# Kernel tuning notes

Measured on AMD Instinct MI355X. Metric: run time of the kernel, lower is better.

## Reference

```python
import jax, jax.numpy as jnp
import numpy as np

N_NODES = 50000


def graph_conv(src, dst, x, W, b, n_nodes):
    """DGL GraphConv, norm='both': D_out^{-1/2} A D_in^{-1/2} x W + b.
    src/dst: [E] edge endpoints (message flows src -> dst).
    """
    ones = jnp.ones(src.shape[0], dtype=x.dtype)
    deg_out = jnp.clip(jax.ops.segment_sum(ones, src, num_segments=n_nodes), 1.0)
    deg_in = jnp.clip(jax.ops.segment_sum(ones, dst, num_segments=n_nodes), 1.0)
    h = x * jax.lax.rsqrt(deg_out)[:, None]          # src-side normalization
    msgs = h[src]                                     # [E, F] gather (irregular)
    agg = jax.ops.segment_sum(msgs, dst, num_segments=n_nodes)  # SpMM scatter-add
    agg = agg * jax.lax.rsqrt(deg_in)[:, None]        # dst-side normalization
    return agg @ W + b


def setup_inputs() -> dict:
    key = jax.random.key(0)
    ks = jax.random.split(key, 9)
    E = 600000
    in_f, hid, emb = 128, 64, 32
    features = jax.random.normal(ks[0], (N_NODES, in_f), dtype=jnp.float32)
    src = jax.random.randint(ks[1], (E,), 0, N_NODES)
    dst = jax.random.randint(ks[2], (E,), 0, N_NODES)

    def glorot(k, fan_in, fan_out):
        lim = np.sqrt(6.0 / (fan_in + fan_out)).astype(np.float32)
        return jax.random.uniform(k, (fan_in, fan_out), jnp.float32, -lim, lim)

    return {
        "features": features, "src": src, "dst": dst,
        "W1": glorot(ks[3], in_f, hid), "b1": jnp.zeros((hid,), jnp.float32),
        "W2": glorot(ks[4], hid, emb), "b2": jnp.zeros((emb,), jnp.float32),
        "W3": glorot(ks[5], emb, in_f), "b3": jnp.zeros((in_f,), jnp.float32),
    }


def reference(features, src, dst, W1, b1, W2, b2, W3, b3):
    h = jax.nn.relu(graph_conv(src, dst, features, W1, b1, N_NODES))
    z = graph_conv(src, dst, h, W2, b2, N_NODES)
    recon = graph_conv(src, dst, z, W3, b3, N_NODES)
    return (z, recon)
```

## Files before the change

### kernel.cpp

```cpp
#include <hip/hip_runtime.h>
#include <hip/hip_bf16.h>


#define NN   50000
#define HPB  128
#define FNB  4
#define FBIN 12500
typedef unsigned short u16;

__device__ __forceinline__ float bfhi(unsigned u) {
    unsigned v = u & 0xFFFF0000u;
    return __builtin_bit_cast(float, v);
}
__device__ __forceinline__ float bflo(unsigned u) {
    unsigned v = u << 16;
    return __builtin_bit_cast(float, v);
}
__device__ __forceinline__ unsigned f2bf(float f) {
    unsigned u = __builtin_bit_cast(unsigned, f);
    return (u + 0x7FFFu + ((u >> 16) & 1u)) >> 16;
}

__global__ __launch_bounds__(256) void k_hist1(
    const int* __restrict__ src, const int* __restrict__ dst,
    u16* __restrict__ slab, int E, int slice)
{
    __shared__ unsigned h[NN / 2];
    const int which = blockIdx.x / HPB;
    const int p     = blockIdx.x % HPB;
    const int* __restrict__ idx = which ? dst : src;

    for (int i = threadIdx.x; i < NN / 2; i += 256) h[i] = 0;
    __syncthreads();

    const int beg = p * slice;
    const int fin = min(beg + slice, E);
    for (int i = beg + threadIdx.x * 4; i + 3 < fin; i += 1024) {
        const int4 v = *(const int4*)(idx + i);
        atomicAdd(&h[v.x >> 1], 1u << ((v.x & 1) << 4));
        atomicAdd(&h[v.y >> 1], 1u << ((v.y & 1) << 4));
        atomicAdd(&h[v.z >> 1], 1u << ((v.z & 1) << 4));
        atomicAdd(&h[v.w >> 1], 1u << ((v.w & 1) << 4));
    }
    for (int i = beg + ((fin - beg) & ~3) + threadIdx.x; i < fin; i += 256) {
        const int u = idx[i];
        atomicAdd(&h[u >> 1], 1u << ((u & 1) << 4));
    }
    __syncthreads();

    unsigned* out = (unsigned*)(slab + (size_t)blockIdx.x * NN);
    for (int i = threadIdx.x; i < NN / 2; i += 256) out[i] = h[i];
}

__global__ __launch_bounds__(256) void k_reduce_scan(
    u16* __restrict__ slab, float* __restrict__ rs_out, float* __restrict__ rs_in,
    int* __restrict__ partial, int* __restrict__ blocksum, int N)
{
    __shared__ int tmp[256];
    const int tid = threadIdx.x;
    const int i = blockIdx.x * 256 + tid;

    int run = 0;
    if (i < N) {
        const u16* s_src = slab + i;
        u16*       s_dst = slab + (size_t)HPB * NN + i;
        int so = 0;
#pragma unroll 8
        for (int p = 0; p < HPB; ++p) so += s_src[(size_t)p * NN];
#pragma unroll 8
        for (int p = 0; p < HPB; ++p) {
            const int c = s_dst[(size_t)p * NN];
            s_dst[(size_t)p * NN] = (u16)run;
            run += c;
        }
        rs_out[i] = rsqrtf(fmaxf((float)so, 1.0f));
        rs_in[i]  = rsqrtf(fmaxf((float)run, 1.0f));
    }
    tmp[tid] = run; __syncthreads();
    for (int off = 1; off < 256; off <<= 1) {
        int t = (tid >= off) ? tmp[tid - off] : 0;
        __syncthreads(); tmp[tid] += t; __syncthreads();
    }
    if (i < N) partial[i] = tmp[tid];
    if (tid == 255) blocksum[blockIdx.x] = tmp[255];
}

__global__ __launch_bounds__(256) void k_scan23(
    const int* __restrict__ partial, const int* __restrict__ blocksum,
    int* __restrict__ row_ptr, int n, int nb)
{
    __shared__ int tmp[256];
    const int tid = threadIdx.x;
    int v = (tid < nb) ? blocksum[tid] : 0;
    tmp[tid] = v; __syncthreads();
    for (int off = 1; off < 256; off <<= 1) {
        int t = (tid >= off) ? tmp[tid - off] : 0;
        __syncthreads(); tmp[tid] += t; __syncthreads();
    }
    __syncthreads();
    const int i = blockIdx.x * 256 + tid;
    if (i < n) {
        const int base = (blockIdx.x > 0) ? tmp[blockIdx.x - 1] : 0;
        row_ptr[i + 1] = partial[i] + base;
        if (i == 0) row_ptr[0] = 0;
    }
}

__global__ __launch_bounds__(256) void k_fill2(
    const int* __restrict__ src, const int* __restrict__ dst,
    const int* __restrict__ row_ptr, const u16* __restrict__ slab,
    int* __restrict__ csr_src, int E, int slice, int N)
{
    __shared__ int cur[FBIN];
    const int bin = blockIdx.x / HPB;
    const int p   = blockIdx.x % HPB;
    const int lo  = bin * FBIN;

    const u16* part_off = slab + (size_t)(HPB + p) * NN;
    for (int j = threadIdx.x; j < FBIN; j += 256) {
        const int node = lo + j;
        cur[j] = (node < N) ? (row_ptr[node] + (int)part_off[node]) : 0;
    }
    __syncthreads();

    const int beg = p * slice;
    const int fin = min(beg + slice, E);
    for (int i = beg + threadIdx.x * 4; i + 3 < fin; i += 1024) {
        const int4 d = *(const int4*)(dst + i);
        const int4 s = *(const int4*)(src + i);
        int u;
        u = d.x - lo; if ((unsigned)u < (unsigned)FBIN) csr_src[atomicAdd(&cur[u], 1)] = s.x;
        u = d.y - lo; if ((unsigned)u < (unsigned)FBIN) csr_src[atomicAdd(&cur[u], 1)] = s.y;
        u = d.z - lo; if ((unsigned)u < (unsigned)FBIN) csr_src[atomicAdd(&cur[u], 1)] = s.z;
        u = d.w - lo; if ((unsigned)u < (unsigned)FBIN) csr_src[atomicAdd(&cur[u], 1)] = s.w;
    }
    for (int i = beg + ((fin - beg) & ~3) + threadIdx.x; i < fin; i += 256) {
        int u = dst[i] - lo;
        if ((unsigned)u < (unsigned)FBIN) csr_src[atomicAdd(&cur[u], 1)] = src[i];
    }
}

template <int IN_F, int OUT_F, int TM>
__global__ __launch_bounds__(256) void k_gemm_bf16out(
    const float* __restrict__ X, const float* __restrict__ W,
    const float* __restrict__ rowscale, u16* __restrict__ Y, int n)
{
    constexpr int CT  = OUT_F / 4;
    constexpr int RT  = 256 / CT;
    constexpr int RPT = TM / RT;
    constexpr int XS  = IN_F + 4;
    __shared__ float sW[IN_F * OUT_F];
    __shared__ float sX[TM * XS];
    const int tid = threadIdx.x;
    const int row0 = blockIdx.x * TM;

    for (int i = tid; i < IN_F * OUT_F / 4; i += 256)
        ((float4*)sW)[i] = ((const float4*)W)[i];
    for (int i = tid; i < TM * IN_F / 4; i += 256) {
        const int r  = i / (IN_F / 4);
        const int c4 = (i % (IN_F / 4)) * 4;
        const int gr = row0 + r;
        float4 v = make_float4(0.f, 0.f, 0.f, 0.f);
        if (gr < n) v = *(const float4*)(X + (long)gr * IN_F + c4);
        *(float4*)(sX + r * XS + c4) = v;
    }
    __syncthreads();

    const int tc = tid % CT;
    const int tr = tid / CT;
    float4 acc[RPT];
#pragma unroll
    for (int i = 0; i < RPT; ++i) acc[i] = make_float4(0.f, 0.f, 0.f, 0.f);

#pragma unroll 8
    for (int k = 0; k < IN_F; ++k) {
        const float4 w = *(const float4*)(sW + k * OUT_F + 4 * tc);
#pragma unroll
        for (int i = 0; i < RPT; ++i) {
            const float xv = sX[(tr + i * RT) * XS + k];
            acc[i].x += xv * w.x; acc[i].y += xv * w.y;
            acc[i].z += xv * w.z; acc[i].w += xv * w.w;
        }
    }

#pragma unroll
    for (int i = 0; i < RPT; ++i) {
        const int gr = row0 + tr + i * RT;
        if (gr < n) {
            float4 v = acc[i];
            const float s = rowscale[gr];
            v.x *= s; v.y *= s; v.z *= s; v.w *= s;
            uint2 pk;
            pk.x = f2bf(v.x) | (f2bf(v.y) << 16);
            pk.y = f2bf(v.z) | (f2bf(v.w) << 16);
            *(uint2*)(Y + (size_t)gr * OUT_F + 4 * tc) = pk;
        }
    }
}

#define ACC8(q) do { \
    a[0] += bflo((q).x); a[1] += bfhi((q).x); a[2] += bflo((q).y); a[3] += bfhi((q).y); \
    a[4] += bflo((q).z); a[5] += bfhi((q).z); a[6] += bflo((q).w); a[7] += bfhi((q).w); } while (0)

__global__ __launch_bounds__(256) void k_gather_gemm_B(
    const int* __restrict__ row_ptr, const int* __restrict__ csr_src,
    const u16* __restrict__ t1b, const float* __restrict__ rs_in,
    const float* __restrict__ rs_out, const float* __restrict__ b1,
    const float* __restrict__ W2, u16* __restrict__ t2b, int N)
{
    __shared__ float sh[16][72];
    __shared__ float sW[64 * 32];
    const int tid = threadIdx.x;

    for (int i = tid; i < 64 * 32 / 4; i += 256)
        ((float4*)sW)[i] = ((const float4*)W2)[i];

    const int nloc = tid >> 4;
    const int sub  = tid & 15;
    const int half = sub >> 3;
    const int c8   = (sub & 7) * 8;
    const int node = blockIdx.x * 16 + nloc;

    float a[8];
#pragma unroll
    for (int t = 0; t < 8; ++t) a[t] = 0.f;

    if (node < N) {
        const int beg = row_ptr[node];
        const int end = row_ptr[node + 1];
        const int len0 = (end - beg + 1) >> 1;
        int j        = half ? beg + len0 : beg;
        const int je = half ? end : beg + len0;
        for (; j + 3 < je; j += 4) {
            const int s0 = csr_src[j], s1 = csr_src[j + 1];
            const int s2 = csr_src[j + 2], s3 = csr_src[j + 3];
            const uint4 q0 = *(const uint4*)(t1b + (size_t)s0 * 64 + c8);
            const uint4 q1 = *(const uint4*)(t1b + (size_t)s1 * 64 + c8);
            const uint4 q2 = *(const uint4*)(t1b + (size_t)s2 * 64 + c8);
            const uint4 q3 = *(const uint4*)(t1b + (size_t)s3 * 64 + c8);
            ACC8(q0); ACC8(q1); ACC8(q2); ACC8(q3);
        }
        for (; j < je; ++j) {
            const uint4 q = *(const uint4*)(t1b + (size_t)csr_src[j] * 64 + c8);
            ACC8(q);
        }
    }
#pragma unroll
    for (int t = 0; t < 8; ++t) a[t] += __shfl_xor(a[t], 8);

    if (node < N && half == 0) {
        const float rs = rs_in[node];
#pragma unroll
        for (int t = 0; t < 8; ++t)
            sh[nloc][c8 + t] = fmaxf(a[t] * rs + b1[c8 + t], 0.f);
    }
    __syncthreads();

    if (tid < 128) {
        const int n2 = tid >> 3;
        const int c4 = (tid & 7) * 4;
        float4 acc = make_float4(0.f, 0.f, 0.f, 0.f);
#pragma unroll 8
        for (int k = 0; k < 64; ++k) {
            const float xv = sh[n2][k];
            const float4 w = *(const float4*)(sW + k * 32 + c4);
            acc.x += xv * w.x; acc.y += xv * w.y; acc.z += xv * w.z; acc.w += xv * w.w;
        }
        const int gn = blockIdx.x * 16 + n2;
        if (gn < N) {
            const float s = rs_out[gn];
            uint2 pk;
            pk.x = f2bf(acc.x * s) | (f2bf(acc.y * s) << 16);
            pk.y = f2bf(acc.z * s) | (f2bf(acc.w * s) << 16);
            *(uint2*)(t2b + (size_t)gn * 32 + c4) = pk;
        }
    }
}

__global__ __launch_bounds__(256) void k_gather_C(
    const int* __restrict__ row_ptr, const int* __restrict__ csr_src,
    const u16* __restrict__ t2b, const float* __restrict__ rs_in,
    const float* __restrict__ rs_out, const float* __restrict__ b2,
    float* __restrict__ z, u16* __restrict__ zb, int N)
{
    const int node = blockIdx.x * 32 + (threadIdx.x >> 3);
    const int sub  = threadIdx.x & 7;
    const int half = sub >> 2;
    const int c8   = (sub & 3) * 8;
    if (node >= N) return;

    const int beg = row_ptr[node];
    const int end = row_ptr[node + 1];
    const int len0 = (end - beg + 1) >> 1;
    int j        = half ? beg + len0 : beg;
    const int je = half ? end : beg + len0;

    float a[8];
#pragma unroll
    for (int t = 0; t < 8; ++t) a[t] = 0.f;

    for (; j + 3 < je; j += 4) {
        const int s0 = csr_src[j], s1 = csr_src[j + 1];
        const int s2 = csr_src[j + 2], s3 = csr_src[j + 3];
        const uint4 q0 = *(const uint4*)(t2b + (size_t)s0 * 32 + c8);
        const uint4 q1 = *(const uint4*)(t2b + (size_t)s1 * 32 + c8);
        const uint4 q2 = *(const uint4*)(t2b + (size_t)s2 * 32 + c8);
        const uint4 q3 = *(const uint4*)(t2b + (size_t)s3 * 32 + c8);
        ACC8(q0); ACC8(q1); ACC8(q2); ACC8(q3);
    }
    for (; j < je; ++j) {
        const uint4 q = *(const uint4*)(t2b + (size_t)csr_src[j] * 32 + c8);
        ACC8(q);
    }
#pragma unroll
    for (int t = 0; t < 8; ++t) a[t] += __shfl_xor(a[t], 4);
    if (half) return;

    const float rs = rs_in[node];
    float v[8];
#pragma unroll
    for (int t = 0; t < 8; ++t) v[t] = a[t] * rs + b2[c8 + t];

    float* o = z + (size_t)node * 32 + c8;
    *(float4*)(o)     = make_float4(v[0], v[1], v[2], v[3]);
    *(float4*)(o + 4) = make_float4(v[4], v[5], v[6], v[7]);

    const float ss = rs_out[node];
    uint4 pk;
    pk.x = f2bf(v[0] * ss) | (f2bf(v[1] * ss) << 16);
    pk.y = f2bf(v[2] * ss) | (f2bf(v[3] * ss) << 16);
    pk.z = f2bf(v[4] * ss) | (f2bf(v[5] * ss) << 16);
    pk.w = f2bf(v[6] * ss) | (f2bf(v[7] * ss) << 16);
    *(uint4*)(zb + (size_t)node * 32 + c8) = pk;
}

__global__ __launch_bounds__(256) void k_gather_gemm_D(
    const int* __restrict__ row_ptr, const int* __restrict__ csr_src,
    const u16* __restrict__ zb, const float* __restrict__ rs_in,
    const float* __restrict__ W3, const float* __restrict__ b3,
    float* __restrict__ recon, int N)
{
    __shared__ float sa[32][36];
    __shared__ float sW[32 * 128];
    const int tid = threadIdx.x;

    for (int i = tid; i < 32 * 128 / 4; i += 256)
        ((float4*)sW)[i] = ((const float4*)W3)[i];

    const int nloc = tid >> 3;
    const int sub  = tid & 7;
    const int half = sub >> 2;
    const int c8   = (sub & 3) * 8;
    const int node = blockIdx.x * 32 + nloc;

    float a[8];
#pragma unroll
    for (int t = 0; t < 8; ++t) a[t] = 0.f;

    if (node < N) {
        const int beg = row_ptr[node];
        const int end = row_ptr[node + 1];
        const int len0 = (end - beg + 1) >> 1;
        int j        = half ? beg + len0 : beg;
        const int je = half ? end : beg + len0;
        for (; j + 3 < je; j += 4) {
            const int s0 = csr_src[j], s1 = csr_src[j + 1];
            const int s2 = csr_src[j + 2], s3 = csr_src[j + 3];
            const uint4 q0 = *(const uint4*)(zb + (size_t)s0 * 32 + c8);
            const uint4 q1 = *(const uint4*)(zb + (size_t)s1 * 32 + c8);
            const uint4 q2 = *(const uint4*)(zb + (size_t)s2 * 32 + c8);
            const uint4 q3 = *(const uint4*)(zb + (size_t)s3 * 32 + c8);
            ACC8(q0); ACC8(q1); ACC8(q2); ACC8(q3);
        }
        for (; j < je; ++j) {
            const uint4 q = *(const uint4*)(zb + (size_t)csr_src[j] * 32 + c8);
            ACC8(q);
        }
    }
#pragma unroll
    for (int t = 0; t < 8; ++t) a[t] += __shfl_xor(a[t], 4);

    if (node < N && half == 0) {
        const float rs = rs_in[node];
#pragma unroll
        for (int t = 0; t < 8; ++t) sa[nloc][c8 + t] = a[t] * rs;
    }
    __syncthreads();

    const int ng = (tid >> 5) * 4;
    const int c4 = (tid & 31) * 4;
    const float4 bb = *(const float4*)(b3 + c4);
    float4 acc[4];
#pragma unroll
    for (int i = 0; i < 4; ++i) acc[i] = bb;
#pragma unroll 4
    for (int k = 0; k < 32; ++k) {
        const float4 w = *(const float4*)(sW + k * 128 + c4);
#pragma unroll
        for (int i = 0; i < 4; ++i) {
            const float xv = sa[ng + i][k];
            acc[i].x += xv * w.x; acc[i].y += xv * w.y;
            acc[i].z += xv * w.z; acc[i].w += xv * w.w;
        }
    }
#pragma unroll
    for (int i = 0; i < 4; ++i) {
        const int gn = blockIdx.x * 32 + ng + i;
        if (gn < N) *(float4*)(recon + (size_t)gn * 128 + c4) = acc[i];
    }
}

extern "C" void kernel_launch(void* const* d_in, const int* in_sizes, int n_in,
                              void* d_out, int out_size, void* d_ws, size_t ws_size,
                              hipStream_t stream) {
    const float* feat = (const float*)d_in[0];
    const int*   src  = (const int*)d_in[1];
    const int*   dst  = (const int*)d_in[2];
    const float* W1   = (const float*)d_in[3];
    const float* b1   = (const float*)d_in[4];
    const float* W2   = (const float*)d_in[5];
    const float* b2   = (const float*)d_in[6];
    const float* W3   = (const float*)d_in[7];
    const float* b3   = (const float*)d_in[8];

    const int E = in_sizes[1];
    const int N = in_sizes[0] / 128;
    const int slice = (((E + HPB - 1) / HPB) + 3) & ~3;

    const size_t SLABN = 2UL * HPB * NN;
    u16* slab     = (u16*)d_ws;
    int* row_ptr  = (int*)(slab + SLABN);
    int* scan_p   = row_ptr + N + 16;
    int* blocksum = scan_p + N;
    int* csr_src  = blocksum + 256;
    float* rs_out = (float*)(csr_src + E);
    float* rs_in  = rs_out + N;
    u16* t2b      = (u16*)(rs_in + N);
    u16* zb       = t2b + (size_t)N * 32;
    u16* t1b      = (u16*)slab;

    float* z_out  = (float*)d_out;
    float* recon  = z_out + (size_t)N * 32;

    const int B = 256;
    const int nb_scan = (N + 255) / 256;

    k_hist1<<<2 * HPB, B, 0, stream>>>(src, dst, slab, E, slice);
    k_reduce_scan<<<nb_scan, B, 0, stream>>>(slab, rs_out, rs_in, scan_p, blocksum, N);
    k_scan23<<<nb_scan, B, 0, stream>>>(scan_p, blocksum, row_ptr, N, nb_scan);
    k_fill2<<<FNB * HPB, B, 0, stream>>>(src, dst, row_ptr, slab, csr_src, E, slice, N);

    k_gemm_bf16out<128, 64, 32><<<(N + 31) / 32, B, 0, stream>>>(
        feat, W1, rs_out, t1b, N);

    k_gather_gemm_B<<<(N + 15) / 16, B, 0, stream>>>(
        row_ptr, csr_src, t1b, rs_in, rs_out, b1, W2, t2b, N);

    k_gather_C<<<(N + 31) / 32, B, 0, stream>>>(
        row_ptr, csr_src, t2b, rs_in, rs_out, b2, z_out, zb, N);

    k_gather_gemm_D<<<(N + 31) / 32, B, 0, stream>>>(
        row_ptr, csr_src, zb, rs_in, W3, b3, recon, N);
}
```

Baseline: 202.5 us.

## Compress CSR to u16 indices with padded rows and quarter-split gathers

Shrinks the per-partition histogram slab from u16 to u8 counters and stores CSR source indices as u16. Each row is padded to a multiple of 16 using a sentinel index (50000) that points at zeroed dummy rows, so gather loops run without tail handling. The gathers are split across four thread groups per node instead of two. This cuts index bandwidth and shared-memory use and lets fill run with two bins instead of four. The cost is that it relies on node ids fitting in 16 bits and per-partition counts fitting in 8 bits, and padding adds wasted gathers.

```diff
diff --git a/kernel.cpp b/kernel.cpp
--- a/kernel.cpp
+++ b/kernel.cpp
@@ -4,9 +4,10 @@
 
 #define NN   50000
 #define HPB  128
-#define FNB  4
-#define FBIN 12500
+#define FNB  2
+#define FBIN 25000
 typedef unsigned short u16;
+typedef unsigned char  u8;
 
 __device__ __forceinline__ float bfhi(unsigned u) {
     unsigned v = u & 0xFFFF0000u;
@@ -23,38 +24,39 @@
 
 __global__ __launch_bounds__(256) void k_hist1(
     const int* __restrict__ src, const int* __restrict__ dst,
-    u16* __restrict__ slab, int E, int slice)
-{
-    __shared__ unsigned h[NN / 2];
+    u8* __restrict__ slab, int E, int slice)
+{
+    __shared__ unsigned h[NN / 4];
     const int which = blockIdx.x / HPB;
     const int p     = blockIdx.x % HPB;
     const int* __restrict__ idx = which ? dst : src;
 
-    for (int i = threadIdx.x; i < NN / 2; i += 256) h[i] = 0;
+    for (int i = threadIdx.x; i < NN / 4; i += 256) h[i] = 0;
     __syncthreads();
 
     const int beg = p * slice;
     const int fin = min(beg + slice, E);
     for (int i = beg + threadIdx.x * 4; i + 3 < fin; i += 1024) {
         const int4 v = *(const int4*)(idx + i);
-        atomicAdd(&h[v.x >> 1], 1u << ((v.x & 1) << 4));
-        atomicAdd(&h[v.y >> 1], 1u << ((v.y & 1) << 4));
-        atomicAdd(&h[v.z >> 1], 1u << ((v.z & 1) << 4));
-        atomicAdd(&h[v.w >> 1], 1u << ((v.w & 1) << 4));
+        atomicAdd(&h[v.x >> 2], 1u << ((v.x & 3) << 3));
+        atomicAdd(&h[v.y >> 2], 1u << ((v.y & 3) << 3));
+        atomicAdd(&h[v.z >> 2], 1u << ((v.z & 3) << 3));
+        atomicAdd(&h[v.w >> 2], 1u << ((v.w & 3) << 3));
     }
     for (int i = beg + ((fin - beg) & ~3) + threadIdx.x; i < fin; i += 256) {
         const int u = idx[i];
-        atomicAdd(&h[u >> 1], 1u << ((u & 1) << 4));
+        atomicAdd(&h[u >> 2], 1u << ((u & 3) << 3));
     }
     __syncthreads();
 
     unsigned* out = (unsigned*)(slab + (size_t)blockIdx.x * NN);
-    for (int i = threadIdx.x; i < NN / 2; i += 256) out[i] = h[i];
+    for (int i = threadIdx.x; i < NN / 4; i += 256) out[i] = h[i];
 }
 
 __global__ __launch_bounds__(256) void k_reduce_scan(
-    u16* __restrict__ slab, float* __restrict__ rs_out, float* __restrict__ rs_in,
-    int* __restrict__ partial, int* __restrict__ blocksum, int N)
+    u8* __restrict__ slab, float* __restrict__ rs_out, float* __restrict__ rs_in,
+    int* __restrict__ partial, int* __restrict__ blocksum,
+    unsigned* __restrict__ csr_words, int ncw, int N)
 {
     __shared__ int tmp[256];
     const int tid = threadIdx.x;
@@ -62,32 +64,36 @@
 
     int run = 0;
     if (i < N) {
-        const u16* s_src = slab + i;
-        u16*       s_dst = slab + (size_t)HPB * NN + i;
+        const u8* s_src = slab + i;
+        u8*       s_dst = slab + (size_t)HPB * NN + i;
         int so = 0;
 #pragma unroll 8
         for (int p = 0; p < HPB; ++p) so += s_src[(size_t)p * NN];
 #pragma unroll 8
         for (int p = 0; p < HPB; ++p) {
             const int c = s_dst[(size_t)p * NN];
-            s_dst[(size_t)p * NN] = (u16)run;
+            s_dst[(size_t)p * NN] = (u8)run;
             run += c;
         }
         rs_out[i] = rsqrtf(fmaxf((float)so, 1.0f));
         rs_in[i]  = rsqrtf(fmaxf((float)run, 1.0f));
     }
-    tmp[tid] = run; __syncthreads();
+    const int pad = (run + 15) & ~15;
+    tmp[tid] = pad; __syncthreads();
     for (int off = 1; off < 256; off <<= 1) {
         int t = (tid >= off) ? tmp[tid - off] : 0;
         __syncthreads(); tmp[tid] += t; __syncthreads();
     }
     if (i < N) partial[i] = tmp[tid];
     if (tid == 255) blocksum[blockIdx.x] = tmp[255];
+
+    for (int w = blockIdx.x * 256 + tid; w < ncw; w += gridDim.x * 256)
+        csr_words[w] = 0xC350C350u;
 }
 
 __global__ __launch_bounds__(256) void k_scan23(
     const int* __restrict__ partial, const int* __restrict__ blocksum,
-    int* __restrict__ row_ptr, int n, int nb)
+    int* __restrict__ row_start, int n, int nb)
 {
     __shared__ int tmp[256];
     const int tid = threadIdx.x;
@@ -101,25 +107,25 @@
     const int i = blockIdx.x * 256 + tid;
     if (i < n) {
         const int base = (blockIdx.x > 0) ? tmp[blockIdx.x - 1] : 0;
-        row_ptr[i + 1] = partial[i] + base;
-        if (i == 0) row_ptr[0] = 0;
+        row_start[i + 1] = partial[i] + base;
+        if (i == 0) row_start[0] = 0;
     }
 }
 
 __global__ __launch_bounds__(256) void k_fill2(
     const int* __restrict__ src, const int* __restrict__ dst,
-    const int* __restrict__ row_ptr, const u16* __restrict__ slab,
-    int* __restrict__ csr_src, int E, int slice, int N)
+    const int* __restrict__ row_start, const u8* __restrict__ slab,
+    u16* __restrict__ csr, int E, int slice, int N)
 {
     __shared__ int cur[FBIN];
     const int bin = blockIdx.x / HPB;
     const int p   = blockIdx.x % HPB;
     const int lo  = bin * FBIN;
 
-    const u16* part_off = slab + (size_t)(HPB + p) * NN;
+    const u8* part_off = slab + (size_t)(HPB + p) * NN;
     for (int j = threadIdx.x; j < FBIN; j += 256) {
         const int node = lo + j;
-        cur[j] = (node < N) ? (row_ptr[node] + (int)part_off[node]) : 0;
+        cur[j] = row_start[node] + (int)part_off[node];
     }
     __syncthreads();
 
@@ -129,21 +135,22 @@
         const int4 d = *(const int4*)(dst + i);
         const int4 s = *(const int4*)(src + i);
         int u;
-        u = d.x - lo; if ((unsigned)u < (unsigned)FBIN) csr_src[atomicAdd(&cur[u], 1)] = s.x;
-        u = d.y - lo; if ((unsigned)u < (unsigned)FBIN) csr_src[atomicAdd(&cur[u], 1)] = s.y;
-        u = d.z - lo; if ((unsigned)u < (unsigned)FBIN) csr_src[atomicAdd(&cur[u], 1)] = s.z;
-        u = d.w - lo; if ((unsigned)u < (unsigned)FBIN) csr_src[atomicAdd(&cur[u], 1)] = s.w;
+        u = d.x - lo; if ((unsigned)u < (unsigned)FBIN) csr[atomicAdd(&cur[u], 1)] = (u16)s.x;
+        u = d.y - lo; if ((unsigned)u < (unsigned)FBIN) csr[atomicAdd(&cur[u], 1)] = (u16)s.y;
+        u = d.z - lo; if ((unsigned)u < (unsigned)FBIN) csr[atomicAdd(&cur[u], 1)] = (u16)s.z;
+        u = d.w - lo; if ((unsigned)u < (unsigned)FBIN) csr[atomicAdd(&cur[u], 1)] = (u16)s.w;
     }
     for (int i = beg + ((fin - beg) & ~3) + threadIdx.x; i < fin; i += 256) {
         int u = dst[i] - lo;
-        if ((unsigned)u < (unsigned)FBIN) csr_src[atomicAdd(&cur[u], 1)] = src[i];
+        if ((unsigned)u < (unsigned)FBIN) csr[atomicAdd(&cur[u], 1)] = (u16)src[i];
     }
 }
 
 template <int IN_F, int OUT_F, int TM>
 __global__ __launch_bounds__(256) void k_gemm_bf16out(
     const float* __restrict__ X, const float* __restrict__ W,
-    const float* __restrict__ rowscale, u16* __restrict__ Y, int n)
+    const float* __restrict__ rowscale, u16* __restrict__ Y,
+    u16* __restrict__ t2b, u16* __restrict__ zb, int n)
 {
     constexpr int CT  = OUT_F / 4;
     constexpr int RT  = 256 / CT;
@@ -153,6 +160,12 @@
     __shared__ float sX[TM * XS];
     const int tid = threadIdx.x;
     const int row0 = blockIdx.x * TM;
+
+    if (blockIdx.x == 0) {
+        if (tid < 32)      ((unsigned*)(Y   + (size_t)NN * 64))[tid]      = 0;
+        else if (tid < 48) ((unsigned*)(t2b + (size_t)NN * 32))[tid - 32] = 0;
+        else if (tid < 64) ((unsigned*)(zb  + (size_t)NN * 32))[tid - 48] = 0;
+    }
 
     for (int i = tid; i < IN_F * OUT_F / 4; i += 256)
         ((float4*)sW)[i] = ((const float4*)W)[i];
@@ -199,56 +212,56 @@
 }
 
 #define ACC8(q) do { \
-    a[0] += bflo((q).x); a[1] += bfhi((q).x); a[2] += bflo((q).y); a[3] += bfhi((q).y); \
-    a[4] += bflo((q).z); a[5] += bfhi((q).z); a[6] += bflo((q).w); a[7] += bfhi((q).w); } while (0)
+    a[0] += bflo((q).x); a[1] += bfhi((q).x); a[2] += bflo((q).y); a[3] += bfhi(q.y); \
+    a[4] += bflo((q).z); a[5] += bfhi((q).z); a[6] += bflo((q).w); a[7] += bfhi(q.w); } while (0)
+
+#define GATHER4(SRCB, RW) do { \
+    const uint2 w = *(const uint2*)(csr + j); \
+    const int s0 = w.x & 0xFFFF, s1 = w.x >> 16; \
+    const int s2 = w.y & 0xFFFF, s3 = w.y >> 16; \
+    const uint4 q0 = *(const uint4*)(SRCB + (size_t)s0 * RW + c8); \
+    const uint4 q1 = *(const uint4*)(SRCB + (size_t)s1 * RW + c8); \
+    const uint4 q2 = *(const uint4*)(SRCB + (size_t)s2 * RW + c8); \
+    const uint4 q3 = *(const uint4*)(SRCB + (size_t)s3 * RW + c8); \
+    ACC8(q0); ACC8(q1); ACC8(q2); ACC8(q3); } while (0)
 
 __global__ __launch_bounds__(256) void k_gather_gemm_B(
-    const int* __restrict__ row_ptr, const int* __restrict__ csr_src,
+    const int* __restrict__ row_start, const u16* __restrict__ csr,
     const u16* __restrict__ t1b, const float* __restrict__ rs_in,
     const float* __restrict__ rs_out, const float* __restrict__ b1,
     const float* __restrict__ W2, u16* __restrict__ t2b, int N)
 {
-    __shared__ float sh[16][72];
+    __shared__ float sh[8][72];
     __shared__ float sW[64 * 32];
     const int tid = threadIdx.x;
 
     for (int i = tid; i < 64 * 32 / 4; i += 256)
         ((float4*)sW)[i] = ((const float4*)W2)[i];
 
-    const int nloc = tid >> 4;
-    const int sub  = tid & 15;
-    const int half = sub >> 3;
+    const int nloc = tid >> 5;
+    const int sub  = tid & 31;
+    const int qtr  = sub >> 3;
     const int c8   = (sub & 7) * 8;
-    const int node = blockIdx.x * 16 + nloc;
+    const int node = blockIdx.x * 8 + nloc;
 
     float a[8];
 #pragma unroll
     for (int t = 0; t < 8; ++t) a[t] = 0.f;
 
     if (node < N) {
-        const int beg = row_ptr[node];
-        const int end = row_ptr[node + 1];
-        const int len0 = (end - beg + 1) >> 1;
-        int j        = half ? beg + len0 : beg;
-        const int je = half ? end : beg + len0;
-        for (; j + 3 < je; j += 4) {
-            const int s0 = csr_src[j], s1 = csr_src[j + 1];
-            const int s2 = csr_src[j + 2], s3 = csr_src[j + 3];
-            const uint4 q0 = *(const uint4*)(t1b + (size_t)s0 * 64 + c8);
-            const uint4 q1 = *(const uint4*)(t1b + (size_t)s1 * 64 + c8);
-            const uint4 q2 = *(const uint4*)(t1b + (size_t)s2 * 64 + c8);
-            const uint4 q3 = *(const uint4*)(t1b + (size_t)s3 * 64 + c8);
-            ACC8(q0); ACC8(q1); ACC8(q2); ACC8(q3);
-        }
-        for (; j < je; ++j) {
-            const uint4 q = *(const uint4*)(t1b + (size_t)csr_src[j] * 64 + c8);
-            ACC8(q);
-        }
-    }
-#pragma unroll
-    for (int t = 0; t < 8; ++t) a[t] += __shfl_xor(a[t], 8);
-
-    if (node < N && half == 0) {
+        const int beg  = row_start[node];
+        const int qlen = (row_start[node + 1] - beg) >> 2;
+        const int j0 = beg + qtr * qlen;
+        const int j1 = j0 + qlen;
+        for (int j = j0; j < j1; j += 4) GATHER4(t1b, 64);
+    }
+#pragma unroll
+    for (int t = 0; t < 8; ++t) {
+        a[t] += __shfl_xor(a[t], 8);
+        a[t] += __shfl_xor(a[t], 16);
+    }
+
+    if (node < N && qtr == 0) {
         const float rs = rs_in[node];
 #pragma unroll
         for (int t = 0; t < 8; ++t)
@@ -256,7 +269,7 @@
     }
     __syncthreads();
 
-    if (tid < 128) {
+    if (tid < 64) {
         const int n2 = tid >> 3;
         const int c4 = (tid & 7) * 4;
         float4 acc = make_float4(0.f, 0.f, 0.f, 0.f);
@@ -266,7 +279,7 @@
             const float4 w = *(const float4*)(sW + k * 32 + c4);
             acc.x += xv * w.x; acc.y += xv * w.y; acc.z += xv * w.z; acc.w += xv * w.w;
         }
-        const int gn = blockIdx.x * 16 + n2;
+        const int gn = blockIdx.x * 8 + n2;
         if (gn < N) {
             const float s = rs_out[gn];
             uint2 pk;
@@ -278,43 +291,33 @@
 }
 
 __global__ __launch_bounds__(256) void k_gather_C(
-    const int* __restrict__ row_ptr, const int* __restrict__ csr_src,
+    const int* __restrict__ row_start, const u16* __restrict__ csr,
     const u16* __restrict__ t2b, const float* __restrict__ rs_in,
     const float* __restrict__ rs_out, const float* __restrict__ b2,
     float* __restrict__ z, u16* __restrict__ zb, int N)
 {
-    const int node = blockIdx.x * 32 + (threadIdx.x >> 3);
-    const int sub  = threadIdx.x & 7;
-    const int half = sub >> 2;
+    const int node = blockIdx.x * 16 + (threadIdx.x >> 4);
+    const int sub  = threadIdx.x & 15;
+    const int qtr  = sub >> 2;
     const int c8   = (sub & 3) * 8;
     if (node >= N) return;
 
-    const int beg = row_ptr[node];
-    const int end = row_ptr[node + 1];
-    const int len0 = (end - beg + 1) >> 1;
-    int j        = half ? beg + len0 : beg;
-    const int je = half ? end : beg + len0;
+    const int beg  = row_start[node];
+    const int qlen = (row_start[node + 1] - beg) >> 2;
+    const int j0 = beg + qtr * qlen;
+    const int j1 = j0 + qlen;
 
     float a[8];
 #pragma unroll
     for (int t = 0; t < 8; ++t) a[t] = 0.f;
-
-    for (; j + 3 < je; j += 4) {
-        const int s0 = csr_src[j], s1 = csr_src[j + 1];
-        const int s2 = csr_src[j + 2], s3 = csr_src[j + 3];
-        const uint4 q0 = *(const uint4*)(t2b + (size_t)s0 * 32 + c8);
-        const uint4 q1 = *(const uint4*)(t2b + (size_t)s1 * 32 + c8);
-        const uint4 q2 = *(const uint4*)(t2b + (size_t)s2 * 32 + c8);
-        const uint4 q3 = *(const uint4*)(t2b + (size_t)s3 * 32 + c8);
-        ACC8(q0); ACC8(q1); ACC8(q2); ACC8(q3);
-    }
-    for (; j < je; ++j) {
-        const uint4 q = *(const uint4*)(t2b + (size_t)csr_src[j] * 32 + c8);
-        ACC8(q);
-    }
-#pragma unroll
-    for (int t = 0; t < 8; ++t) a[t] += __shfl_xor(a[t], 4);
-    if (half) return;
+    for (int j = j0; j < j1; j += 4) GATHER4(t2b, 32);
+
+#pragma unroll
+    for (int t = 0; t < 8; ++t) {
+        a[t] += __shfl_xor(a[t], 4);
+        a[t] += __shfl_xor(a[t], 8);
+    }
+    if (qtr) return;
 
     const float rs = rs_in[node];
     float v[8];
@@ -335,77 +338,66 @@
 }
 
 __global__ __launch_bounds__(256) void k_gather_gemm_D(
-    const int* __restrict__ row_ptr, const int* __restrict__ csr_src,
+    const int* __restrict__ row_start, const u16* __restrict__ csr,
     const u16* __restrict__ zb, const float* __restrict__ rs_in,
     const float* __restrict__ W3, const float* __restrict__ b3,
     float* __restrict__ recon, int N)
 {
-    __shared__ float sa[32][36];
+    __shared__ float sa[16][36];
     __shared__ float sW[32 * 128];
     const int tid = threadIdx.x;
 
     for (int i = tid; i < 32 * 128 / 4; i += 256)
         ((float4*)sW)[i] = ((const float4*)W3)[i];
 
-    const int nloc = tid >> 3;
-    const int sub  = tid & 7;
-    const int half = sub >> 2;
+    const int nloc = tid >> 4;
+    const int sub  = tid & 15;
+    const int qtr  = sub >> 2;
     const int c8   = (sub & 3) * 8;
-    const int node = blockIdx.x * 32 + nloc;
+    const int node = blockIdx.x * 16 + nloc;
 
     float a[8];
 #pragma unroll
     for (int t = 0; t < 8; ++t) a[t] = 0.f;
 
     if (node < N) {
-        const int beg = row_ptr[node];
-        const int end = row_ptr[node + 1];
-        const int len0 = (end - beg + 1) >> 1;
-        int j        = half ? beg + len0 : beg;
-        const int je = half ? end : beg + len0;
-        for (; j + 3 < je; j += 4) {
-            const int s0 = csr_src[j], s1 = csr_src[j + 1];
-            const int s2 = csr_src[j + 2], s3 = csr_src[j + 3];
-            const uint4 q0 = *(const uint4*)(zb + (size_t)s0 * 32 + c8);
-            const uint4 q1 = *(const uint4*)(zb + (size_t)s1 * 32 + c8);
-            const uint4 q2 = *(const uint4*)(zb + (size_t)s2 * 32 + c8);
-            const uint4 q3 = *(const uint4*)(zb + (size_t)s3 * 32 + c8);
-            ACC8(q0); ACC8(q1); ACC8(q2); ACC8(q3);
-        }
-        for (; j < je; ++j) {
-            const uint4 q = *(const uint4*)(zb + (size_t)csr_src[j] * 32 + c8);
-            ACC8(q);
-        }
-    }
-#pragma unroll
-    for (int t = 0; t < 8; ++t) a[t] += __shfl_xor(a[t], 4);
-
-    if (node < N && half == 0) {
+        const int beg  = row_start[node];
+        const int qlen = (row_start[node + 1] - beg) >> 2;
+        const int j0 = beg + qtr * qlen;
+        const int j1 = j0 + qlen;
+        for (int j = j0; j < j1; j += 4) GATHER4(zb, 32);
+    }
+#pragma unroll
+    for (int t = 0; t < 8; ++t) {
+        a[t] += __shfl_xor(a[t], 4);
+        a[t] += __shfl_xor(a[t], 8);
+    }
+
+    if (node < N && qtr == 0) {
         const float rs = rs_in[node];
 #pragma unroll
         for (int t = 0; t < 8; ++t) sa[nloc][c8 + t] = a[t] * rs;
     }
     __syncthreads();
 
-    const int ng = (tid >> 5) * 4;
+    const int ng = (tid >> 5) * 2;
     const int c4 = (tid & 31) * 4;
     const float4 bb = *(const float4*)(b3 + c4);
-    float4 acc[4];
-#pragma unroll
-    for (int i = 0; i < 4; ++i) acc[i] = bb;
+    float4 acc[2];
+    acc[0] = bb; acc[1] = bb;
 #pragma unroll 4
     for (int k = 0; k < 32; ++k) {
         const float4 w = *(const float4*)(sW + k * 128 + c4);
 #pragma unroll
-        for (int i = 0; i < 4; ++i) {
+        for (int i = 0; i < 2; ++i) {
             const float xv = sa[ng + i][k];
             acc[i].x += xv * w.x; acc[i].y += xv * w.y;
             acc[i].z += xv * w.z; acc[i].w += xv * w.w;
         }
     }
 #pragma unroll
-    for (int i = 0; i < 4; ++i) {
-        const int gn = blockIdx.x * 32 + ng + i;
+    for (int i = 0; i < 2; ++i) {
+        const int gn = blockIdx.x * 16 + ng + i;
         if (gn < N) *(float4*)(recon + (size_t)gn * 128 + c4) = acc[i];
     }
 }
@@ -426,17 +418,19 @@
     const int E = in_sizes[1];
     const int N = in_sizes[0] / 128;
     const int slice = (((E + HPB - 1) / HPB) + 3) & ~3;
-
-    const size_t SLABN = 2UL * HPB * NN;
-    u16* slab     = (u16*)d_ws;
-    int* row_ptr  = (int*)(slab + SLABN);
-    int* scan_p   = row_ptr + N + 16;
+    const int CSRMAX = E + 15 * N;
+    const int ncw = CSRMAX / 2;
+
+    const size_t SLABB = 2UL * HPB * NN;
+    u8*  slab     = (u8*)d_ws;
+    int* row_start= (int*)(slab + SLABB);
+    int* scan_p   = row_start + N + 16;
     int* blocksum = scan_p + N;
-    int* csr_src  = blocksum + 256;
-    float* rs_out = (float*)(csr_src + E);
+    u16* csr      = (u16*)(blocksum + 256);
+    float* rs_out = (float*)(csr + CSRMAX);
     float* rs_in  = rs_out + N;
     u16* t2b      = (u16*)(rs_in + N);
-    u16* zb       = t2b + (size_t)N * 32;
+    u16* zb       = t2b + (size_t)(N + 8) * 32;
     u16* t1b      = (u16*)slab;
 
     float* z_out  = (float*)d_out;
@@ -446,19 +440,20 @@
     const int nb_scan = (N + 255) / 256;
 
     k_hist1<<<2 * HPB, B, 0, stream>>>(src, dst, slab, E, slice);
-    k_reduce_scan<<<nb_scan, B, 0, stream>>>(slab, rs_out, rs_in, scan_p, blocksum, N);
-    k_scan23<<<nb_scan, B, 0, stream>>>(scan_p, blocksum, row_ptr, N, nb_scan);
-    k_fill2<<<FNB * HPB, B, 0, stream>>>(src, dst, row_ptr, slab, csr_src, E, slice, N);
+    k_reduce_scan<<<nb_scan, B, 0, stream>>>(slab, rs_out, rs_in, scan_p, blocksum,
+                                             (unsigned*)csr, ncw, N);
+    k_scan23<<<nb_scan, B, 0, stream>>>(scan_p, blocksum, row_start, N, nb_scan);
+    k_fill2<<<FNB * HPB, B, 0, stream>>>(src, dst, row_start, slab, csr, E, slice, N);
 
     k_gemm_bf16out<128, 64, 32><<<(N + 31) / 32, B, 0, stream>>>(
-        feat, W1, rs_out, t1b, N);
-
-    k_gather_gemm_B<<<(N + 15) / 16, B, 0, stream>>>(
-        row_ptr, csr_src, t1b, rs_in, rs_out, b1, W2, t2b, N);
-
-    k_gather_C<<<(N + 31) / 32, B, 0, stream>>>(
-        row_ptr, csr_src, t2b, rs_in, rs_out, b2, z_out, zb, N);
-
-    k_gather_gemm_D<<<(N + 31) / 32, B, 0, stream>>>(
-        row_ptr, csr_src, zb, rs_in, W3, b3, recon, N);
-}
+        feat, W1, rs_out, t1b, t2b, zb, N);
+
+    k_gather_gemm_B<<<(N + 7) / 8, B, 0, stream>>>(
+        row_start, csr, t1b, rs_in, rs_out, b1, W2, t2b, N);
+
+    k_gather_C<<<(N + 15) / 16, B, 0, stream>>>(
+        row_start, csr, t2b, rs_in, rs_out, b2, z_out, zb, N);
+
+    k_gather_gemm_D<<<(N + 15) / 16, B, 0, stream>>>(
+        row_start, csr, zb, rs_in, W3, b3, recon, N);
+}
```

New measurement: 190.9 us. 1.06x faster.
